# Kernel tuning notes

Measured on AMD Instinct MI355X. Metric: run time of the kernel, lower is better.

## Reference

```python
import jax, jax.numpy as jnp
import numpy as np

NEG_INF = -1e9  # additive mask value for masked softmax


def setup_inputs() -> dict:
    key = jax.random.key(0)
    k1, k2, k3, k4, k5 = jax.random.split(key, 5)
    bz, rv_num, rv_len, in_feat, out_feat = 32, 10, 128, 300, 128
    seq_a = jax.random.normal(k1, (bz, rv_num, rv_len, in_feat), dtype=jnp.float32)
    seq_b = jax.random.normal(k2, (bz, rv_num, rv_len, in_feat), dtype=jnp.float32)
    mask_a = jax.random.randint(k3, (bz, rv_num, rv_len), 0, 2, dtype=jnp.int32)
    mask_b = jax.random.randint(k4, (bz, rv_num, rv_len), 0, 2, dtype=jnp.int32)
    # guarantee at least one valid position per review (avoid fully-masked rows)
    mask_a = mask_a.at[:, :, 0].set(1)
    mask_b = mask_b.at[:, :, 0].set(1)
    # FC transform params (xavier-normal-ish weight, zero bias)
    W = jax.random.normal(k5, (in_feat, out_feat), dtype=jnp.float32) * (2.0 / np.sqrt(in_feat + out_feat))
    b = jnp.zeros((out_feat,), dtype=jnp.float32)
    return {"seq_a": seq_a, "seq_b": seq_b, "mask_a": mask_a, "mask_b": mask_b, "W": W, "b": b}


def _masked_softmax(scores, mask):
    # scores: [N, L], mask: [N, L] in {0,1}
    logits = jnp.where(mask > 0, scores, NEG_INF)
    return jax.nn.softmax(logits, axis=-1)


def reference(seq_a, seq_b, mask_a, mask_b, W, b):
    bz, rv_num, rv_len, _ = seq_a.shape
    hdim = W.shape[1]
    N = bz * rv_num          # flattened batch of reviews
    M = rv_num * rv_len      # all tokens on the other side

    # FC + ReLU feature transform
    ta = jax.nn.relu(jnp.einsum('bnld,dh->bnlh', seq_a, W) + b)
    tb = jax.nn.relu(jnp.einsum('bnld,dh->bnlh', seq_b, W) + b)

    sa = ta.reshape(N, rv_len, hdim)
    sb = tb.reshape(N, rv_len, hdim)
    # expand: each review attends over ALL tokens of the other sequence in its sample
    ea = jnp.broadcast_to(ta.reshape(bz, 1, M, hdim), (bz, rv_num, M, hdim)).reshape(N, M, hdim)
    eb = jnp.broadcast_to(tb.reshape(bz, 1, M, hdim), (bz, rv_num, M, hdim)).reshape(N, M, hdim)

    # DOT interaction (no scale): affinity [N, rv_len, M]
    atob_aff = jnp.einsum('nld,nmd->nlm', sa, eb)
    btoa_aff = jnp.einsum('nld,nmd->nlm', sb, ea)

    # MEAN pooling over the other-sequence axis
    atob_scores = atob_aff.mean(axis=-1)  # [N, rv_len]
    btoa_scores = btoa_aff.mean(axis=-1)

    ma = mask_a.reshape(N, rv_len)
    mb = mask_b.reshape(N, rv_len)
    atob_w = _masked_softmax(atob_scores, ma)
    btoa_w = _masked_softmax(btoa_scores, mb)

    a_out = jnp.einsum('nl,nld->nd', atob_w, sa)
    b_out = jnp.einsum('nl,nld->nd', btoa_w, sb)
    return (a_out, b_out, atob_w, btoa_w)
```

## Files before the change

kernel.cpp:

```cpp
#include <hip/hip_runtime.h>
#include <hip/hip_bf16.h>


#define K_FEAT 300
#define H 128
#define NTOK 40960
#define NREV 320
#define TOK_PER_SAMPLE 1280
#define TM 128
#define BLKS_PER_SAMPLE 10
#define LDA 40
#define NCHUNK 10
#define WFRAG_ELEMS (NCHUNK * 4 * 4 * 64 * 8)

typedef __attribute__((ext_vector_type(8))) short bf16x8;
typedef __attribute__((ext_vector_type(4))) float f32x4;
typedef unsigned short u16;
typedef unsigned int u32;

static __device__ __forceinline__ u16 f2bf(float x) {
    u32 u = __float_as_uint(x);
    return (u16)((u + 0x7fffu + ((u >> 16) & 1u)) >> 16);
}
static __device__ __forceinline__ float bf2f(u16 s) {
    return __uint_as_float(((u32)s) << 16);
}

__global__ void wsplit_kernel(const float* __restrict__ W, u16* __restrict__ Wfrag)
{
    int i = blockIdx.x * 256 + threadIdx.x;
    if (i >= WFRAG_ELEMS) return;
    int j    = i & 7;
    int lane = (i >> 3) & 63;
    int frag = (i >> 9) & 3;
    int wave = (i >> 11) & 3;
    int c    = i >> 13;
    int nn = lane & 15, quad = lane >> 4;
    int t2 = frag >> 1, part = frag & 1;
    int h = (2 * wave + t2) * 16 + nn;
    int k = c * 32 + quad * 8 + j;
    float w = (k < K_FEAT) ? W[(size_t)k * H + h] : 0.f;
    u16 hi = f2bf(w);
    Wfrag[i] = part ? f2bf(w - bf2f(hi)) : hi;
}

__global__ __launch_bounds__(256, 3) void fc_mfma_kernel(
    const float* __restrict__ seq_a, const float* __restrict__ seq_b,
    const u16* __restrict__ Wfrag, const float* __restrict__ bias,
    float* __restrict__ ta, float* __restrict__ tb,
    float* __restrict__ psum_a, float* __restrict__ psum_b)
{
    __shared__ u16 Ah_s[TM * LDA];
    __shared__ u16 Al_s[TM * LDA];
    __shared__ float bias_s[H];

    int blk = blockIdx.x;
    const float* seq; float* outp; float* psum;
    if (blk < 320) { seq = seq_a; outp = ta; psum = psum_a; }
    else           { seq = seq_b; outp = tb; psum = psum_b; blk -= 320; }

    const int tid = threadIdx.x;
    const int tok0 = blk * TM;
    const int wave = tid >> 6;
    const int lane = tid & 63;
    const int nn = lane & 15;
    const int quad = lane >> 4;

    if (tid < H) bias_s[tid] = bias[tid];

    const int st_t = tid >> 3;
    const int st_j = tid & 7;

    f32x4 acc[8][2];
#pragma unroll
    for (int m = 0; m < 8; ++m) {
        acc[m][0] = (f32x4){0.f, 0.f, 0.f, 0.f};
        acc[m][1] = (f32x4){0.f, 0.f, 0.f, 0.f};
    }

    float4 pf[4];
#pragma unroll
    for (int it = 0; it < 4; ++it) {
        int t = st_t + it * 32;
        int kk = 4 * st_j;
        pf[it] = make_float4(0.f, 0.f, 0.f, 0.f);
        if (kk + 4 <= K_FEAT)
            pf[it] = *(const float4*)&seq[(size_t)(tok0 + t) * K_FEAT + kk];
    }
#pragma unroll
    for (int it = 0; it < 4; ++it) {
        int t = st_t + it * 32;
        float4 v = pf[it];
        u16 h0 = f2bf(v.x), h1 = f2bf(v.y), h2 = f2bf(v.z), h3 = f2bf(v.w);
        uint2 hp, lp;
        hp.x = (u32)h0 | ((u32)h1 << 16);
        hp.y = (u32)h2 | ((u32)h3 << 16);
        lp.x = (u32)f2bf(v.x - bf2f(h0)) | ((u32)f2bf(v.y - bf2f(h1)) << 16);
        lp.y = (u32)f2bf(v.z - bf2f(h2)) | ((u32)f2bf(v.w - bf2f(h3)) << 16);
        *(uint2*)&Ah_s[t * LDA + 4 * st_j] = hp;
        *(uint2*)&Al_s[t * LDA + 4 * st_j] = lp;
    }
    __syncthreads();

    for (int c = 0; c < NCHUNK; ++c) {
        if (c < NCHUNK - 1) {
#pragma unroll
            for (int it = 0; it < 4; ++it) {
                int t = st_t + it * 32;
                int kk = (c + 1) * 32 + 4 * st_j;
                pf[it] = make_float4(0.f, 0.f, 0.f, 0.f);
                if (kk + 4 <= K_FEAT)
                    pf[it] = *(const float4*)&seq[(size_t)(tok0 + t) * K_FEAT + kk];
            }
        }
        const u16* wf = Wfrag + (size_t)(c * 4 + wave) * 2048;
        bf16x8 bh0 = *(const bf16x8*)&wf[0 * 512 + lane * 8];
        bf16x8 bl0 = *(const bf16x8*)&wf[1 * 512 + lane * 8];
        bf16x8 bh1 = *(const bf16x8*)&wf[2 * 512 + lane * 8];
        bf16x8 bl1 = *(const bf16x8*)&wf[3 * 512 + lane * 8];
#pragma unroll
        for (int m = 0; m < 8; ++m) {
            bf16x8 a_hi = *(const bf16x8*)&Ah_s[(m * 16 + nn) * LDA + quad * 8];
            bf16x8 a_lo = *(const bf16x8*)&Al_s[(m * 16 + nn) * LDA + quad * 8];
            acc[m][0] = __builtin_amdgcn_mfma_f32_16x16x32_bf16(a_hi, bh0, acc[m][0], 0, 0, 0);
            acc[m][0] = __builtin_amdgcn_mfma_f32_16x16x32_bf16(a_hi, bl0, acc[m][0], 0, 0, 0);
            acc[m][0] = __builtin_amdgcn_mfma_f32_16x16x32_bf16(a_lo, bh0, acc[m][0], 0, 0, 0);
            acc[m][1] = __builtin_amdgcn_mfma_f32_16x16x32_bf16(a_hi, bh1, acc[m][1], 0, 0, 0);
            acc[m][1] = __builtin_amdgcn_mfma_f32_16x16x32_bf16(a_hi, bl1, acc[m][1], 0, 0, 0);
            acc[m][1] = __builtin_amdgcn_mfma_f32_16x16x32_bf16(a_lo, bh1, acc[m][1], 0, 0, 0);
        }
        __syncthreads();
        if (c < NCHUNK - 1) {
#pragma unroll
            for (int it = 0; it < 4; ++it) {
                int t = st_t + it * 32;
                float4 v = pf[it];
                u16 h0 = f2bf(v.x), h1 = f2bf(v.y), h2 = f2bf(v.z), h3 = f2bf(v.w);
                uint2 hp, lp;
                hp.x = (u32)h0 | ((u32)h1 << 16);
                hp.y = (u32)h2 | ((u32)h3 << 16);
                lp.x = (u32)f2bf(v.x - bf2f(h0)) | ((u32)f2bf(v.y - bf2f(h1)) << 16);
                lp.y = (u32)f2bf(v.z - bf2f(h2)) | ((u32)f2bf(v.w - bf2f(h3)) << 16);
                *(uint2*)&Ah_s[t * LDA + 4 * st_j] = hp;
                *(uint2*)&Al_s[t * LDA + 4 * st_j] = lp;
            }
            __syncthreads();
        }
    }

#pragma unroll
    for (int t2 = 0; t2 < 2; ++t2) {
        int hcol = (2 * wave + t2) * 16 + nn;
        float bv = bias_s[hcol];
        float fs = 0.f;
#pragma unroll
        for (int m = 0; m < 8; ++m) {
#pragma unroll
            for (int reg = 0; reg < 4; ++reg) {
                int tok = tok0 + m * 16 + quad * 4 + reg;
                float v = fmaxf(acc[m][t2][reg] + bv, 0.f);
                outp[(size_t)tok * H + hcol] = v;
                fs += v;
            }
        }
        fs += __shfl_xor(fs, 16);
        fs += __shfl_xor(fs, 32);
        if (quad == 0) psum[(size_t)blk * H + hcol] = fs;
    }
}

__global__ __launch_bounds__(256) void attn_kernel(
    const float* __restrict__ ta, const float* __restrict__ tb,
    const int* __restrict__ mask_a, const int* __restrict__ mask_b,
    const float* __restrict__ psum_a, const float* __restrict__ psum_b,
    float* __restrict__ out)
{
    int n = blockIdx.x;
    int side = 0;
    if (n >= NREV) { side = 1; n -= NREV; }

    const float* t = side ? tb : ta;
    const int* mask = side ? mask_b : mask_a;
    const float* psum_o = side ? psum_a : psum_b;
    float* out_vec = out + (side ? NREV * H : 0);
    float* out_w = out + 2 * NREV * H + (side ? NREV * H : 0);

    int sample = n / 10;
    int tid = threadIdx.x;

    __shared__ float score_part[128 * 33];
    __shared__ float mean_s[128];
    __shared__ float w_s[128];
    __shared__ float red[4];
    __shared__ float part_out[8 * 128];

    if (tid < 128) {
        float s = 0.f;
        const float* pb = psum_o + (size_t)sample * BLKS_PER_SAMPLE * H + tid;
#pragma unroll
        for (int i = 0; i < BLKS_PER_SAMPLE; ++i) s += pb[(size_t)i * H];
        mean_s[tid] = s * (1.0f / (float)TOK_PER_SAMPLE);
    }
    __syncthreads();

    const float* rowbase = t + (size_t)n * 128 * H;

#pragma unroll
    for (int i = 0; i < 16; ++i) {
        int q = tid + 256 * i;
        int r = q >> 5;
        int c4 = q & 31;
        float4 v = *(const float4*)&rowbase[q * 4];
        float4 m = *(const float4*)&mean_s[c4 * 4];
        score_part[r * 33 + c4] = v.x * m.x + v.y * m.y + v.z * m.z + v.w * m.w;
    }
    __syncthreads();

    float logit = -1e9f;
    if (tid < 128) {
        float s = 0.f;
#pragma unroll
        for (int j = 0; j < 32; ++j) s += score_part[tid * 33 + j];
        int mv = mask[n * 128 + tid];
        logit = (mv > 0) ? s : -1e9f;
    }

    float mx = logit;
    for (int off = 32; off > 0; off >>= 1) mx = fmaxf(mx, __shfl_xor(mx, off));
    if ((tid & 63) == 0) red[tid >> 6] = mx;
    __syncthreads();
    mx = fmaxf(fmaxf(red[0], red[1]), fmaxf(red[2], red[3]));
    __syncthreads();

    float e = __expf(logit - mx);
    float ssum = e;
    for (int off = 32; off > 0; off >>= 1) ssum += __shfl_xor(ssum, off);
    if ((tid & 63) == 0) red[tid >> 6] = ssum;
    __syncthreads();
    ssum = red[0] + red[1] + red[2] + red[3];

    float w = e / ssum;
    if (tid < 128) {
        w_s[tid] = w;
        out_w[n * 128 + tid] = w;
    }
    __syncthreads();

    int c4 = tid & 31;
    int lp = tid >> 5;
    float4 o4 = make_float4(0.f, 0.f, 0.f, 0.f);
#pragma unroll
    for (int k = 0; k < 16; ++k) {
        int l = k * 8 + lp;
        float wl = w_s[l];
        float4 v = *(const float4*)&rowbase[(size_t)l * H + c4 * 4];
        o4.x = fmaf(wl, v.x, o4.x);
        o4.y = fmaf(wl, v.y, o4.y);
        o4.z = fmaf(wl, v.z, o4.z);
        o4.w = fmaf(wl, v.w, o4.w);
    }
    *(float4*)&part_out[lp * 128 + c4 * 4] = o4;
    __syncthreads();
    if (tid < 128) {
        float o = 0.f;
#pragma unroll
        for (int p = 0; p < 8; ++p) o += part_out[p * 128 + tid];
        out_vec[n * 128 + tid] = o;
    }
}

extern "C" void kernel_launch(void* const* d_in, const int* in_sizes, int n_in,
                              void* d_out, int out_size, void* d_ws, size_t ws_size,
                              hipStream_t stream)
{
    const float* seq_a = (const float*)d_in[0];
    const float* seq_b = (const float*)d_in[1];
    const int* mask_a = (const int*)d_in[2];
    const int* mask_b = (const int*)d_in[3];
    const float* W = (const float*)d_in[4];
    const float* bias = (const float*)d_in[5];
    float* out = (float*)d_out;

    float* ws = (float*)d_ws;
    float* ta = ws;
    float* tb = ta + (size_t)NTOK * H;
    float* psum_a = tb + (size_t)NTOK * H;
    float* psum_b = psum_a + NREV * H;
    u16* Wfrag = (u16*)(psum_b + NREV * H);

    wsplit_kernel<<<(WFRAG_ELEMS + 255) / 256, 256, 0, stream>>>(W, Wfrag);
    fc_mfma_kernel<<<640, 256, 0, stream>>>(seq_a, seq_b, Wfrag, bias, ta, tb, psum_a, psum_b);
    attn_kernel<<<640, 256, 0, stream>>>(ta, tb, mask_a, mask_b, psum_a, psum_b, out);
}
```

Before: 163.6 us.

## Store FC intermediates as bf16 and transpose MFMA output for vectorized stores

The FC kernel now writes the ReLU-transformed features as bf16 instead of fp32, halving the intermediate write traffic and the attention kernel's reads. The MFMA operands are swapped so each lane holds four consecutive hidden columns, which allows packed 8-byte stores and a reshuffled column-sum reduction. The attention kernel is adapted to read 8 bf16 values per load. Rounding the intermediates to bf16 loses precision in the scores and output vectors, which could exceed the tolerance.

```diff
diff --git a/kernel.cpp b/kernel.cpp
--- a/kernel.cpp
+++ b/kernel.cpp
@@ -47,7 +47,7 @@
 __global__ __launch_bounds__(256, 3) void fc_mfma_kernel(
     const float* __restrict__ seq_a, const float* __restrict__ seq_b,
     const u16* __restrict__ Wfrag, const float* __restrict__ bias,
-    float* __restrict__ ta, float* __restrict__ tb,
+    u16* __restrict__ ta, u16* __restrict__ tb,
     float* __restrict__ psum_a, float* __restrict__ psum_b)
 {
     __shared__ u16 Ah_s[TM * LDA];
@@ -55,7 +55,7 @@
     __shared__ float bias_s[H];
 
     int blk = blockIdx.x;
-    const float* seq; float* outp; float* psum;
+    const float* seq; u16* outp; float* psum;
     if (blk < 320) { seq = seq_a; outp = ta; psum = psum_a; }
     else           { seq = seq_b; outp = tb; psum = psum_b; blk -= 320; }
 
@@ -122,12 +122,12 @@
         for (int m = 0; m < 8; ++m) {
             bf16x8 a_hi = *(const bf16x8*)&Ah_s[(m * 16 + nn) * LDA + quad * 8];
             bf16x8 a_lo = *(const bf16x8*)&Al_s[(m * 16 + nn) * LDA + quad * 8];
-            acc[m][0] = __builtin_amdgcn_mfma_f32_16x16x32_bf16(a_hi, bh0, acc[m][0], 0, 0, 0);
-            acc[m][0] = __builtin_amdgcn_mfma_f32_16x16x32_bf16(a_hi, bl0, acc[m][0], 0, 0, 0);
-            acc[m][0] = __builtin_amdgcn_mfma_f32_16x16x32_bf16(a_lo, bh0, acc[m][0], 0, 0, 0);
-            acc[m][1] = __builtin_amdgcn_mfma_f32_16x16x32_bf16(a_hi, bh1, acc[m][1], 0, 0, 0);
-            acc[m][1] = __builtin_amdgcn_mfma_f32_16x16x32_bf16(a_hi, bl1, acc[m][1], 0, 0, 0);
-            acc[m][1] = __builtin_amdgcn_mfma_f32_16x16x32_bf16(a_lo, bh1, acc[m][1], 0, 0, 0);
+            acc[m][0] = __builtin_amdgcn_mfma_f32_16x16x32_bf16(bh0, a_hi, acc[m][0], 0, 0, 0);
+            acc[m][0] = __builtin_amdgcn_mfma_f32_16x16x32_bf16(bl0, a_hi, acc[m][0], 0, 0, 0);
+            acc[m][0] = __builtin_amdgcn_mfma_f32_16x16x32_bf16(bh0, a_lo, acc[m][0], 0, 0, 0);
+            acc[m][1] = __builtin_amdgcn_mfma_f32_16x16x32_bf16(bh1, a_hi, acc[m][1], 0, 0, 0);
+            acc[m][1] = __builtin_amdgcn_mfma_f32_16x16x32_bf16(bl1, a_hi, acc[m][1], 0, 0, 0);
+            acc[m][1] = __builtin_amdgcn_mfma_f32_16x16x32_bf16(bh1, a_lo, acc[m][1], 0, 0, 0);
         }
         __syncthreads();
         if (c < NCHUNK - 1) {
@@ -149,28 +149,40 @@
     }
 
 #pragma unroll
-    for (int t2 = 0; t2 < 2; ++t2) {
-        int hcol = (2 * wave + t2) * 16 + nn;
-        float bv = bias_s[hcol];
-        float fs = 0.f;
-#pragma unroll
-        for (int m = 0; m < 8; ++m) {
-#pragma unroll
-            for (int reg = 0; reg < 4; ++reg) {
-                int tok = tok0 + m * 16 + quad * 4 + reg;
-                float v = fmaxf(acc[m][t2][reg] + bv, 0.f);
-                outp[(size_t)tok * H + hcol] = v;
-                fs += v;
-            }
-        }
-        fs += __shfl_xor(fs, 16);
-        fs += __shfl_xor(fs, 32);
-        if (quad == 0) psum[(size_t)blk * H + hcol] = fs;
+    for (int ht = 0; ht < 2; ++ht) {
+        int h0 = (2 * wave + ht) * 16 + quad * 4;
+        float4 bb = *(const float4*)&bias_s[h0];
+        float fs[4] = {0.f, 0.f, 0.f, 0.f};
+#pragma unroll
+        for (int tt = 0; tt < 8; ++tt) {
+            int tok = tok0 + tt * 16 + nn;
+            float v0 = fmaxf(acc[tt][ht][0] + bb.x, 0.f);
+            float v1 = fmaxf(acc[tt][ht][1] + bb.y, 0.f);
+            float v2 = fmaxf(acc[tt][ht][2] + bb.z, 0.f);
+            float v3 = fmaxf(acc[tt][ht][3] + bb.w, 0.f);
+            fs[0] += v0; fs[1] += v1; fs[2] += v2; fs[3] += v3;
+            uint2 p;
+            p.x = (u32)f2bf(v0) | ((u32)f2bf(v1) << 16);
+            p.y = (u32)f2bf(v2) | ((u32)f2bf(v3) << 16);
+            *(uint2*)&outp[(size_t)tok * H + h0] = p;
+        }
+#pragma unroll
+        for (int r = 0; r < 4; ++r) {
+            fs[r] += __shfl_xor(fs[r], 1);
+            fs[r] += __shfl_xor(fs[r], 2);
+            fs[r] += __shfl_xor(fs[r], 4);
+            fs[r] += __shfl_xor(fs[r], 8);
+        }
+        if (nn == 0) {
+#pragma unroll
+            for (int r = 0; r < 4; ++r)
+                psum[(size_t)blk * H + h0 + r] = fs[r];
+        }
     }
 }
 
 __global__ __launch_bounds__(256) void attn_kernel(
-    const float* __restrict__ ta, const float* __restrict__ tb,
+    const u16* __restrict__ ta, const u16* __restrict__ tb,
     const int* __restrict__ mask_a, const int* __restrict__ mask_b,
     const float* __restrict__ psum_a, const float* __restrict__ psum_b,
     float* __restrict__ out)
@@ -179,7 +191,7 @@
     int side = 0;
     if (n >= NREV) { side = 1; n -= NREV; }
 
-    const float* t = side ? tb : ta;
+    const u16* t = side ? tb : ta;
     const int* mask = side ? mask_b : mask_a;
     const float* psum_o = side ? psum_a : psum_b;
     float* out_vec = out + (side ? NREV * H : 0);
@@ -188,11 +200,11 @@
     int sample = n / 10;
     int tid = threadIdx.x;
 
-    __shared__ float score_part[128 * 33];
+    __shared__ float score_part[128 * 17];
     __shared__ float mean_s[128];
     __shared__ float w_s[128];
     __shared__ float red[4];
-    __shared__ float part_out[8 * 128];
+    __shared__ float part_out[16 * 128];
 
     if (tid < 128) {
         float s = 0.f;
@@ -203,16 +215,25 @@
     }
     __syncthreads();
 
-    const float* rowbase = t + (size_t)n * 128 * H;
-
-#pragma unroll
-    for (int i = 0; i < 16; ++i) {
+    const u16* rowbase = t + (size_t)n * 128 * H;
+
+#pragma unroll
+    for (int i = 0; i < 8; ++i) {
         int q = tid + 256 * i;
-        int r = q >> 5;
-        int c4 = q & 31;
-        float4 v = *(const float4*)&rowbase[q * 4];
-        float4 m = *(const float4*)&mean_s[c4 * 4];
-        score_part[r * 33 + c4] = v.x * m.x + v.y * m.y + v.z * m.z + v.w * m.w;
+        int r = q >> 4;
+        int c8 = q & 15;
+        uint4 v = *(const uint4*)&rowbase[r * H + c8 * 8];
+        const float* m = &mean_s[c8 * 8];
+        float p = 0.f;
+        p += bf2f((u16)(v.x & 0xffff)) * m[0];
+        p += bf2f((u16)(v.x >> 16)) * m[1];
+        p += bf2f((u16)(v.y & 0xffff)) * m[2];
+        p += bf2f((u16)(v.y >> 16)) * m[3];
+        p += bf2f((u16)(v.z & 0xffff)) * m[4];
+        p += bf2f((u16)(v.z >> 16)) * m[5];
+        p += bf2f((u16)(v.w & 0xffff)) * m[6];
+        p += bf2f((u16)(v.w >> 16)) * m[7];
+        score_part[r * 17 + c8] = p;
     }
     __syncthreads();
 
@@ -220,7 +241,7 @@
     if (tid < 128) {
         float s = 0.f;
 #pragma unroll
-        for (int j = 0; j < 32; ++j) s += score_part[tid * 33 + j];
+        for (int j = 0; j < 16; ++j) s += score_part[tid * 17 + j];
         int mv = mask[n * 128 + tid];
         logit = (mv > 0) ? s : -1e9f;
     }
@@ -246,26 +267,31 @@
     }
     __syncthreads();
 
-    int c4 = tid & 31;
-    int lp = tid >> 5;
-    float4 o4 = make_float4(0.f, 0.f, 0.f, 0.f);
-#pragma unroll
-    for (int k = 0; k < 16; ++k) {
-        int l = k * 8 + lp;
+    int c8 = tid & 15;
+    int lp = tid >> 4;
+    float o[8] = {0.f, 0.f, 0.f, 0.f, 0.f, 0.f, 0.f, 0.f};
+#pragma unroll
+    for (int k = 0; k < 8; ++k) {
+        int l = k * 16 + lp;
         float wl = w_s[l];
-        float4 v = *(const float4*)&rowbase[(size_t)l * H + c4 * 4];
-        o4.x = fmaf(wl, v.x, o4.x);
-        o4.y = fmaf(wl, v.y, o4.y);
-        o4.z = fmaf(wl, v.z, o4.z);
-        o4.w = fmaf(wl, v.w, o4.w);
-    }
-    *(float4*)&part_out[lp * 128 + c4 * 4] = o4;
+        uint4 v = *(const uint4*)&rowbase[l * H + c8 * 8];
+        o[0] = fmaf(wl, bf2f((u16)(v.x & 0xffff)), o[0]);
+        o[1] = fmaf(wl, bf2f((u16)(v.x >> 16)), o[1]);
+        o[2] = fmaf(wl, bf2f((u16)(v.y & 0xffff)), o[2]);
+        o[3] = fmaf(wl, bf2f((u16)(v.y >> 16)), o[3]);
+        o[4] = fmaf(wl, bf2f((u16)(v.z & 0xffff)), o[4]);
+        o[5] = fmaf(wl, bf2f((u16)(v.z >> 16)), o[5]);
+        o[6] = fmaf(wl, bf2f((u16)(v.w & 0xffff)), o[6]);
+        o[7] = fmaf(wl, bf2f((u16)(v.w >> 16)), o[7]);
+    }
+    *(float4*)&part_out[lp * 128 + c8 * 8] = make_float4(o[0], o[1], o[2], o[3]);
+    *(float4*)&part_out[lp * 128 + c8 * 8 + 4] = make_float4(o[4], o[5], o[6], o[7]);
     __syncthreads();
     if (tid < 128) {
-        float o = 0.f;
-#pragma unroll
-        for (int p = 0; p < 8; ++p) o += part_out[p * 128 + tid];
-        out_vec[n * 128 + tid] = o;
+        float s = 0.f;
+#pragma unroll
+        for (int p = 0; p < 16; ++p) s += part_out[p * 128 + tid];
+        out_vec[n * 128 + tid] = s;
     }
 }
 
@@ -281,10 +307,9 @@
     const float* bias = (const float*)d_in[5];
     float* out = (float*)d_out;
 
-    float* ws = (float*)d_ws;
-    float* ta = ws;
-    float* tb = ta + (size_t)NTOK * H;
-    float* psum_a = tb + (size_t)NTOK * H;
+    u16* ta = (u16*)d_ws;
+    u16* tb = ta + (size_t)NTOK * H;
+    float* psum_a = (float*)(tb + (size_t)NTOK * H);
     float* psum_b = psum_a + NREV * H;
     u16* Wfrag = (u16*)(psum_b + NREV * H);
 
```

Measured after the change: 162.0 us. Within noise of the previous version (-1.0%).
